# Optimization experiments

Hardware: AMD Instinct MI355X
Metric: run time of the kernel (lower is better)

Reference implementation:

```python
import jax, jax.numpy as jnp
import numpy as np

B, L, C, V = 16, 600, 256, 256
OUT_SEQ = 6000
KSZ = 5
DILATIONS = (1, 2, 4)
N_BLOCKS = 10
COND = 256  # speaker(128) + noise(128)
TEMP = 10.0
EPS = 1e-5


def _ccbn(x, cond, gw, gb, bw, bb):
    # x: (B, C, L); conditional batch-norm: per-channel stats over (batch, length),
    # gamma/beta predicted from condition vector.
    mu = jnp.mean(x, axis=(0, 2), keepdims=True)
    var = jnp.var(x, axis=(0, 2), keepdims=True)
    xn = (x - mu) * jax.lax.rsqrt(var + EPS)
    gamma = 1.0 + cond @ gw + gb  # (B, C)
    beta = cond @ bw + bb         # (B, C)
    return xn * gamma[:, :, None] + beta[:, :, None]


def _conv1d(x, w, b, dil=1):
    # x: (B, C_in, L); w: (C_out, C_in, K)
    y = jax.lax.conv_general_dilated(
        x, w, window_strides=(1,), padding='SAME', rhs_dilation=(dil,),
        dimension_numbers=('NCH', 'OIH', 'NCH'))
    return y + b[None, :, None]


def setup_inputs() -> dict:
    key = jax.random.key(0)
    ks = jax.random.split(key, 20)
    s = 0.02
    inp = {
        'inputs': jax.random.randint(ks[0], (B, L), 0, V),
        'speaker_embeddings': jax.random.normal(ks[1], (B, 128), jnp.float32),
        'noise': jax.random.normal(ks[2], (B, 128), jnp.float32),
        'emb': jax.random.normal(ks[3], (V, C), jnp.float32) * s,
        # 10 blocks x 3 dilated convs
        'conv_w': jax.random.normal(ks[4], (N_BLOCKS, 3, C, C, KSZ), jnp.float32) * s,
        'conv_b': jnp.zeros((N_BLOCKS, 3, C), jnp.float32),
        # CCBN projections per conv (gamma/beta from condition)
        'g_w': jax.random.normal(ks[5], (N_BLOCKS, 3, COND, C), jnp.float32) * s,
        'g_b': jnp.zeros((N_BLOCKS, 3, C), jnp.float32),
        'b_w': jax.random.normal(ks[6], (N_BLOCKS, 3, COND, C), jnp.float32) * s,
        'b_b': jnp.zeros((N_BLOCKS, 3, C), jnp.float32),
        # TokenLength head: 2 CCBNs + conv1 (256->256,k1) + conv2 (256->1,k1)
        'tl_g_w': jax.random.normal(ks[7], (2, COND, C), jnp.float32) * s,
        'tl_g_b': jnp.zeros((2, C), jnp.float32),
        'tl_b_w': jax.random.normal(ks[8], (2, COND, C), jnp.float32) * s,
        'tl_b_b': jnp.zeros((2, C), jnp.float32),
        'tl_conv1_w': jax.random.normal(ks[9], (C, C, 1), jnp.float32) * s,
        'tl_conv1_b': jnp.zeros((C,), jnp.float32),
        'tl_conv2_w': jax.random.normal(ks[10], (1, C, 1), jnp.float32) * s,
        'tl_conv2_b': jnp.zeros((1,), jnp.float32),
    }
    return inp


def reference(inputs, speaker_embeddings, noise, emb, conv_w, conv_b,
              g_w, g_b, b_w, b_b, tl_g_w, tl_g_b, tl_b_w, tl_b_b,
              tl_conv1_w, tl_conv1_b, tl_conv2_w, tl_conv2_b):
    cond = jnp.concatenate([speaker_embeddings, noise], axis=-1)  # (B, COND)
    x = emb[inputs]                    # (B, L, C)
    x = jnp.transpose(x, (0, 2, 1))    # (B, C, L)

    # 10 unaligned blocks: residual stacks of CCBN -> ReLU -> dilated conv
    for blk in range(N_BLOCKS):
        y = x
        for j, d in enumerate(DILATIONS):
            y = jax.nn.relu(_ccbn(y, cond, g_w[blk, j], g_b[blk, j], b_w[blk, j], b_b[blk, j]))
            y = _conv1d(y, conv_w[blk, j], conv_b[blk, j], dil=d)
        x = x + y
    unaligned = x  # (B, C, L)

    # TokenLength head
    t = jax.nn.relu(_ccbn(unaligned, cond, tl_g_w[0], tl_g_b[0], tl_b_w[0], tl_b_b[0]))
    t = _conv1d(t, tl_conv1_w, tl_conv1_b)
    t = jax.nn.relu(_ccbn(t, cond, tl_g_w[1], tl_g_b[1], tl_b_w[1], tl_b_b[1]))
    t = _conv1d(t, tl_conv2_w, tl_conv2_b)  # (B, 1, L)
    token_lengths = jax.nn.relu(t[:, 0, :])  # (B, L)

    token_ends = jnp.cumsum(token_lengths, axis=-1)        # (B, L)
    token_centers = token_ends - token_lengths / 2.0        # (B, L)
    aligned_lengths = token_ends

    out_pos = jnp.arange(OUT_SEQ, dtype=jnp.float32)         # (OUT,)
    diff = token_centers[:, None, :] - out_pos[None, :, None]  # (B, OUT, L)
    logits = -(diff * diff) / TEMP
    weights = jax.nn.softmax(logits, axis=-1)                # (B, OUT, L)

    feats = jnp.transpose(unaligned, (0, 2, 1))              # (B, L, C)
    aligned_features = jnp.einsum('bol,blc->boc', weights, feats)  # (B, OUT, C)
    return aligned_features, aligned_lengths
```

## Files before the change

### kernel.cpp

```cpp
#include <hip/hip_runtime.h>
#include <math.h>
#include <stdint.h>

#define EPSv 1e-5f

typedef short short8 __attribute__((ext_vector_type(8)));
typedef float floatx4 __attribute__((ext_vector_type(4)));

__device__ __forceinline__ unsigned short f2bf(float x) {
  unsigned u = __float_as_uint(x);
  unsigned r = (u + 0x7fffu + ((u >> 16) & 1u)) >> 16;
  return (unsigned short)r;
}

__device__ __forceinline__ void gld_lds16(const void* g, void* l) {
  __builtin_amdgcn_global_load_lds(
      (const __attribute__((address_space(1))) unsigned*)(uintptr_t)g,
      (__attribute__((address_space(3))) unsigned*)(uintptr_t)l,
      16, 0, 0);
}

__global__ __launch_bounds__(256) void k_gb_part(const float* __restrict__ spk,
                             const float* __restrict__ noise,
                             const float* __restrict__ g_w, const float* __restrict__ b_w,
                             const float* __restrict__ tl_g_w, const float* __restrict__ tl_b_w,
                             float* __restrict__ gpart, float* __restrict__ bpart) {
  __shared__ float condl[16][32];
  int i = blockIdx.x, ks = blockIdx.y;
  int t = threadIdx.x;
  for (int idx = t; idx < 512; idx += 256) {
    int b = idx >> 5, kk = idx & 31;
    int k = ks*32 + kk;
    condl[b][kk] = (k < 128) ? spk[b*128 + k] : noise[b*128 + k - 128];
  }
  __syncthreads();
  const float *gw, *bw;
  if (i < 30) { gw = g_w + (size_t)i*65536; bw = b_w + (size_t)i*65536; }
  else        { gw = tl_g_w + (size_t)(i-30)*65536; bw = tl_b_w + (size_t)(i-30)*65536; }
  int co = t;
  float g[16], bt[16];
  #pragma unroll
  for (int b = 0; b < 16; ++b) { g[b] = 0.f; bt[b] = 0.f; }
  for (int kk = 0; kk < 32; ++kk) {
    float gwv = gw[(size_t)(ks*32 + kk)*256 + co];
    float bwv = bw[(size_t)(ks*32 + kk)*256 + co];
    #pragma unroll
    for (int b = 0; b < 16; ++b) {
      float cv = condl[b][kk];
      g[b]  = fmaf(cv, gwv, g[b]);
      bt[b] = fmaf(cv, bwv, bt[b]);
    }
  }
  size_t base = ((size_t)(i*8 + ks)*16)*256 + co;
  #pragma unroll
  for (int b = 0; b < 16; ++b) {
    gpart[base + (size_t)b*256] = g[b];
    bpart[base + (size_t)b*256] = bt[b];
  }
}

__global__ void k_gb_red(const float* __restrict__ gpart, const float* __restrict__ bpart,
                         const float* __restrict__ g_b, const float* __restrict__ b_b,
                         const float* __restrict__ tl_g_b, const float* __restrict__ tl_b_b,
                         float* __restrict__ gammas, float* __restrict__ betas) {
  int idx = blockIdx.x*256 + threadIdx.x;
  int i = idx >> 12, rem = idx & 4095;
  int co = rem & 255;
  float gs = 0.f, bs = 0.f;
  #pragma unroll
  for (int ks = 0; ks < 8; ++ks) {
    size_t p = ((size_t)(i*8 + ks) << 12) + rem;
    gs += gpart[p];
    bs += bpart[p];
  }
  float gbias = (i < 30) ? g_b[i*256 + co] : tl_g_b[(i-30)*256 + co];
  float bbias = (i < 30) ? b_b[i*256 + co] : tl_b_b[(i-30)*256 + co];
  gammas[idx] = 1.0f + gs + gbias;
  betas [idx] = bs + bbias;
}

template<int TAPS>
__device__ __forceinline__ void wprep_body(const float* __restrict__ src,
                                           unsigned short* __restrict__ dst,
                                           int cotile, int chunk, int t) {
  int cow = t >> 2, ci8 = (t & 3) * 8;
  const float* s0 = src + ((size_t)(cotile*64 + cow)*256 + chunk*32 + ci8)*TAPS;
  float v[8*TAPS];
  #pragma unroll
  for (int i = 0; i < 8*TAPS; ++i) v[i] = s0[i];
  unsigned short* dblk = dst + (size_t)cotile*(8*TAPS*4096) + (size_t)chunk*(TAPS*4096);
  #pragma unroll
  for (int tap = 0; tap < TAPS; ++tap) {
    unsigned hi2[4], lo2[4];
    #pragma unroll
    for (int jj = 0; jj < 4; ++jj) {
      float a = v[(jj*2+0)*TAPS + tap], b = v[(jj*2+1)*TAPS + tap];
      unsigned short ha = f2bf(a), hb = f2bf(b);
      unsigned short la = f2bf(a - __uint_as_float((unsigned)ha << 16));
      unsigned short lb = f2bf(b - __uint_as_float((unsigned)hb << 16));
      hi2[jj] = (unsigned)ha | ((unsigned)hb << 16);
      lo2[jj] = (unsigned)la | ((unsigned)lb << 16);
    }
    uint4 H; H.x = hi2[0]; H.y = hi2[1]; H.z = hi2[2]; H.w = hi2[3];
    uint4 L; L.x = lo2[0]; L.y = lo2[1]; L.z = lo2[2]; L.w = lo2[3];
    *(uint4*)(dblk + (size_t)(tap*2)*2048 + cow*32 + ci8) = H;
    *(uint4*)(dblk + (size_t)(tap*2+1)*2048 + cow*32 + ci8) = L;
  }
}

__global__ __launch_bounds__(256) void k_wprep(const float* __restrict__ conv_w,
                                               const float* __restrict__ tl_c1_w,
                                               unsigned short* __restrict__ wp) {
  int cc = blockIdx.x;
  int cotile = blockIdx.y >> 3, chunk = blockIdx.y & 7;
  if (cc == 30) wprep_body<1>(tl_c1_w, wp + (size_t)30*655360, cotile, chunk, threadIdx.x);
  else          wprep_body<5>(conv_w + (size_t)cc*327680, wp + (size_t)cc*655360, cotile, chunk, threadIdx.x);
}

__global__ void k_embed2(const int* __restrict__ inp, const float* __restrict__ emb,
                         float* __restrict__ x, float* __restrict__ statp) {
  int bx = blockIdx.x;
  int c = threadIdx.x;
  int r0 = bx * 120;
  float s = 0.f, s2 = 0.f;
  for (int r = 0; r < 120; ++r) {
    int row = inp[r0 + r];
    float v = emb[(size_t)row*256 + c];
    x[(size_t)(r0 + r)*256 + c] = v;
    s += v; s2 = fmaf(v, v, s2);
  }
  statp[(size_t)bx*512 + c] = s;
  statp[(size_t)bx*512 + 256 + c] = s2;
}

__global__ __launch_bounds__(256) void k_norm(const float* __restrict__ z,
                      const float* __restrict__ statp,
                      const float* __restrict__ gam, const float* __restrict__ bet,
                      unsigned short* __restrict__ zn) {
  __shared__ float s_sc[32];
  __shared__ float s_sh[32];
  __shared__ float red[2][32][8];
  int b = blockIdx.x, chunk = blockIdx.y, sub = blockIdx.z;
  int t = threadIdx.x;
  {
    int ch = t >> 3, g = t & 7;
    int c = chunk*32 + ch;
    float s = 0.f, s2 = 0.f;
    for (int p = g; p < 80; p += 8) {
      s  += statp[(size_t)p*512 + c];
      s2 += statp[(size_t)p*512 + 256 + c];
    }
    red[0][ch][g] = s; red[1][ch][g] = s2;
  }
  __syncthreads();
  if (t < 32) {
    float s = 0.f, s2 = 0.f;
    #pragma unroll
    for (int g = 0; g < 8; ++g) { s += red[0][t][g]; s2 += red[1][t][g]; }
    int c = chunk*32 + t;
    float mu = s * (1.0f/9600.0f);
    float var = s2 * (1.0f/9600.0f) - mu*mu;
    float rs = rsqrtf(var + EPSv);
    float scale = rs * gam[b*256 + c];
    s_sc[t] = scale;
    s_sh[t] = fmaf(-mu, scale, bet[b*256 + c]);
  }
  __syncthreads();
  int srow = t >> 3, fq = t & 7;
  float4 sc4 = *(const float4*)&s_sc[fq*4];
  float4 sh4 = *(const float4*)&s_sh[fq*4];
  unsigned short* zh = zn + ((size_t)b*8 + chunk)*54400 + fq*4;
  unsigned short* zl = zh + 27200;
  const float* zb = z + (size_t)b*600*256 + chunk*32 + fq*4;
  int r0 = sub*68;
  #pragma unroll
  for (int i = 0; i < 3; ++i) {
    int rr = i*32 + srow;
    if (rr < 68) {
      int r = r0 + rr;
      int l = r - 8;
      uint2 vh; vh.x = 0u; vh.y = 0u;
      uint2 vl; vl.x = 0u; vl.y = 0u;
      if (l >= 0 && l < 600) {
        float4 zv = *(const float4*)&zb[(size_t)l*256];
        float v0 = fmaxf(fmaf(zv.x, sc4.x, sh4.x), 0.f);
        float v1 = fmaxf(fmaf(zv.y, sc4.y, sh4.y), 0.f);
        float v2 = fmaxf(fmaf(zv.z, sc4.z, sh4.z), 0.f);
        float v3 = fmaxf(fmaf(zv.w, sc4.w, sh4.w), 0.f);
        unsigned short h0 = f2bf(v0), h1 = f2bf(v1), h2 = f2bf(v2), h3 = f2bf(v3);
        unsigned short e0 = f2bf(v0 - __uint_as_float((unsigned)h0 << 16));
        unsigned short e1 = f2bf(v1 - __uint_as_float((unsigned)h1 << 16));
        unsigned short e2 = f2bf(v2 - __uint_as_float((unsigned)h2 << 16));
        unsigned short e3 = f2bf(v3 - __uint_as_float((unsigned)h3 << 16));
        vh.x = (unsigned)h0 | ((unsigned)h1 << 16);
        vh.y = (unsigned)h2 | ((unsigned)h3 << 16);
        vl.x = (unsigned)e0 | ((unsigned)e1 << 16);
        vl.y = (unsigned)e2 | ((unsigned)e3 << 16);
      }
      *(uint2*)&zh[(size_t)r*40] = vh;
      *(uint2*)&zl[(size_t)r*40] = vl;
    }
  }
}

template<int TAPS>
__global__ __launch_bounds__(256, 3) void k_convm(const unsigned short* __restrict__ zn,
                        float* __restrict__ out, float* __restrict__ statp,
                        const unsigned short* __restrict__ wpc,
                        const float* __restrict__ bias, int dil, int mode) {
  __shared__ __align__(16) unsigned short Zhi[2][6144];
  __shared__ __align__(16) unsigned short Zlo[2][6144];
  __shared__ float lsum[32];
  __shared__ float lsq[32];
  int t = threadIdx.x;
  int bx = blockIdx.x;
  int b  = bx / 5;
  int l0 = (bx % 5) * 128;
  int y = blockIdx.y;
  int co0 = y * 32;
  int cobase = (y & 1) * 32;
  int PAD = ((TAPS - 1)/2) * dil;
  int w = t >> 6, lane = t & 63;
  int lsub = (w & 1) * 64, cosub = (w >> 1) * 16;
  int quad = lane >> 4, nlan = lane & 15;
  if (t < 32) { lsum[t] = 0.f; lsq[t] = 0.f; }

  floatx4 acc[4];
  #pragma unroll
  for (int mt = 0; mt < 4; ++mt) acc[mt] = (floatx4){0.f,0.f,0.f,0.f};

  const unsigned short* zbase = zn + (size_t)b*435200 + (size_t)(l0 - PAD + 8)*40 + (size_t)lane*8;
  int ar[4];
  #pragma unroll
  for (int mt = 0; mt < 4; ++mt) ar[mt] = (lsub + mt*16 + nlan) * 40 + quad * 8;

  #define STAGEZ(ch, bf) do {                                             \
    const unsigned short* srcp = zbase + (size_t)(ch)*54400;              \
    for (int i = w; i < 24; i += 4) {                                     \
      int p = (i >= 12) ? 1 : 0;                                          \
      int k = i - p*12;                                                   \
      gld_lds16(srcp + p*27200 + k*512, (p ? Zlo[bf] : Zhi[bf]) + k*512); \
    }                                                                     \
  } while (0)

  STAGEZ(0, 0);
  __syncthreads();

  for (int chunk = 0; chunk < 8; ++chunk) {
    int cb = chunk & 1;
    if (chunk < 7) STAGEZ(chunk + 1, cb ^ 1);
    const unsigned short* pch = wpc + (size_t)((y >> 1)*8 + chunk) * (TAPS*4096);
    short8 bh[TAPS], bl[TAPS];
    int cw = (cobase + cosub + nlan)*32 + quad*8;
    #pragma unroll
    for (int tap = 0; tap < TAPS; ++tap) {
      bh[tap] = *(const short8*)(pch + (size_t)(tap*2)*2048 + cw);
      bl[tap] = *(const short8*)(pch + (size_t)(tap*2+1)*2048 + cw);
    }
    #pragma unroll
    for (int tap = 0; tap < TAPS; ++tap) {
      int sh = tap * dil * 40;
      #pragma unroll
      for (int mt = 0; mt < 4; ++mt) {
        short8 ah = *(const short8*)&Zhi[cb][ar[mt] + sh];
        short8 al = *(const short8*)&Zlo[cb][ar[mt] + sh];
        acc[mt] = __builtin_amdgcn_mfma_f32_16x16x32_bf16(ah, bh[tap], acc[mt], 0, 0, 0);
        acc[mt] = __builtin_amdgcn_mfma_f32_16x16x32_bf16(ah, bl[tap], acc[mt], 0, 0, 0);
        acc[mt] = __builtin_amdgcn_mfma_f32_16x16x32_bf16(al, bh[tap], acc[mt], 0, 0, 0);
      }
    }
    __syncthreads();
  }
  #undef STAGEZ

  float bsv = bias[co0 + cosub + nlan];
  float ssum = 0.f, ssq = 0.f;
  #pragma unroll
  for (int mt = 0; mt < 4; ++mt) {
    #pragma unroll
    for (int r = 0; r < 4; ++r) {
      int l = l0 + lsub + mt*16 + quad*4 + r;
      if (l < 600) {
        float v = acc[mt][r] + bsv;
        float* dst = &out[((size_t)(b*600 + l))*256 + co0 + cosub + nlan];
        if (mode) v += *dst;
        *dst = v;
        ssum += v;
        ssq = fmaf(v, v, ssq);
      }
    }
  }
  ssum += __shfl_xor(ssum, 16, 64);
  ssum += __shfl_xor(ssum, 32, 64);
  ssq  += __shfl_xor(ssq, 16, 64);
  ssq  += __shfl_xor(ssq, 32, 64);
  if (quad == 0) {
    atomicAdd(&lsum[cosub + nlan], ssum);
    atomicAdd(&lsq [cosub + nlan], ssq);
  }
  __syncthreads();
  if (t < 32) {
    statp[(size_t)bx*512 + co0 + t] = lsum[t];
    statp[(size_t)bx*512 + 256 + co0 + t] = lsq[t];
  }
}

__global__ void k_statred(const float* __restrict__ sp, float* __restrict__ dst) {
  int idx = blockIdx.x*256 + threadIdx.x;
  float s = 0.f;
  for (int p = 0; p < 80; ++p) s += sp[(size_t)p*512 + idx];
  dst[idx] = s;
}

__global__ void k_tl2(const float* __restrict__ z, const float* __restrict__ stat,
                      const float* __restrict__ gam, const float* __restrict__ bet,
                      const float* __restrict__ w2, const float* __restrict__ b2,
                      float* __restrict__ tl) {
  int t = threadIdx.x;
  int row = blockIdx.x * 4 + (t >> 6);
  int lane = t & 63;
  int b = row / 600;
  float4 s1 = *(const float4*)&stat[lane*4];
  float4 s2 = *(const float4*)&stat[256 + lane*4];
  float4 gm = *(const float4*)&gam[b*256 + lane*4];
  float4 bt = *(const float4*)&bet[b*256 + lane*4];
  float sc[4], sh[4];
  {
    float sv[4] = {s1.x, s1.y, s1.z, s1.w};
    float qv[4] = {s2.x, s2.y, s2.z, s2.w};
    float gv[4] = {gm.x, gm.y, gm.z, gm.w};
    float bv[4] = {bt.x, bt.y, bt.z, bt.w};
    #pragma unroll
    for (int i = 0; i < 4; ++i) {
      float mu = sv[i] * (1.0f/9600.0f);
      float var = qv[i] * (1.0f/9600.0f) - mu*mu;
      float rs = rsqrtf(var + EPSv);
      sc[i] = rs * gv[i];
      sh[i] = fmaf(-mu, sc[i], bv[i]);
    }
  }
  float4 zr = *(const float4*)&z[(size_t)row*256 + lane*4];
  float4 wr = *(const float4*)&w2[lane*4];
  float z0 = fmaxf(fmaf(zr.x, sc[0], sh[0]), 0.f);
  float z1 = fmaxf(fmaf(zr.y, sc[1], sh[1]), 0.f);
  float z2 = fmaxf(fmaf(zr.z, sc[2], sh[2]), 0.f);
  float z3 = fmaxf(fmaf(zr.w, sc[3], sh[3]), 0.f);
  float s = z0*wr.x + z1*wr.y + z2*wr.z + z3*wr.w;
  for (int m = 32; m >= 1; m >>= 1) s += __shfl_xor(s, m, 64);
  if (lane == 0) tl[row] = fmaxf(s + b2[0], 0.f);
}

__global__ void k_cumsum(const float* __restrict__ tl, float* __restrict__ centers,
                         float* __restrict__ out_len) {
  int b = blockIdx.x; int lane = threadIdx.x;
  float carry = 0.f;
  for (int ch = 0; ch < 10; ++ch) {
    int l = ch*64 + lane;
    float v = (l < 600) ? tl[b*600 + l] : 0.f;
    float s = v;
    #pragma unroll
    for (int off = 1; off < 64; off <<= 1) {
      float n = __shfl_up(s, off, 64);
      if (lane >= off) s += n;
    }
    float ends = carry + s;
    if (l < 600) {
      centers[b*600 + l] = ends - 0.5f*v;
      out_len[b*600 + l] = ends;
    }
    carry = __shfl(ends, 63, 64);
  }
}

__global__ void k_tobf16(const float* __restrict__ x, unsigned short* __restrict__ fbT) {
  __shared__ unsigned short T[64*66];
  int b = blockIdx.x, lt = blockIdx.y, ct = blockIdx.z;
  int t = threadIdx.x;
  int i4 = t >> 6;
  int j = t & 63;
  #pragma unroll
  for (int r = 0; r < 16; ++r) {
    int li = i4*16 + r;
    int l = lt*64 + li;
    float v = (l < 600) ? x[((size_t)(b*600 + l))*256 + ct*64 + j] : 0.f;
    T[j*66 + li] = f2bf(v);
  }
  __syncthreads();
  int row = t >> 2, seg = (t & 3) * 16;
  unsigned vv[8];
  #pragma unroll
  for (int k = 0; k < 8; ++k)
    vv[k] = *(const unsigned*)&T[row*66 + seg + k*2];
  size_t dsth = ((size_t)(b*256 + ct*64 + row))*640 + lt*64 + seg;
  unsigned* du = (unsigned*)fbT;
  uint4 a; a.x = vv[0]; a.y = vv[1]; a.z = vv[2]; a.w = vv[3];
  uint4 c4; c4.x = vv[4]; c4.y = vv[5]; c4.z = vv[6]; c4.w = vv[7];
  *(uint4*)(du + dsth/2) = a;
  *(uint4*)(du + dsth/2 + 4) = c4;
}

__global__ __launch_bounds__(256, 4) void k_align2(const unsigned short* __restrict__ fbT,
                        const float* __restrict__ centers, float* __restrict__ outp) {
  __shared__ float cen[600];
  __shared__ float mrow[64];
  __shared__ float isum[64];
  __shared__ unsigned short Wt[2][64*80];
  int b = blockIdx.x;
  int o0 = blockIdx.y * 64;
  int t = threadIdx.x;
  int wv = t >> 6, lane = t & 63;
  for (int i = t; i < 600; i += 256) cen[i] = centers[b*600 + i];
  __syncthreads();
  for (int rr = 0; rr < 16; ++rr) {
    int oi = wv*16 + rr;
    float opos = (float)(o0 + oi);
    float mx = -3.0e38f;
    for (int l = lane; l < 600; l += 64) {
      float d = cen[l] - opos;
      mx = fmaxf(mx, -d*d*0.1f);
    }
    #pragma unroll
    for (int mm = 32; mm >= 1; mm >>= 1) mx = fmaxf(mx, __shfl_xor(mx, mm, 64));
    if (lane == 0) mrow[oi] = mx;
  }
  __syncthreads();
  floatx4 acc[4][4];
  #pragma unroll
  for (int i = 0; i < 4; ++i)
    #pragma unroll
    for (int j = 0; j < 4; ++j)
      acc[i][j] = (floatx4){0.f, 0.f, 0.f, 0.f};
  int quad = lane >> 4;
  int nlan = lane & 15;
  int oi_w = t >> 2;
  int sbase = t & 3;
  float mo = mrow[oi_w];
  float opos_w = (float)(o0 + oi_w);
  float psum = 0.f;
  const unsigned short* srcb = fbT + ((size_t)b*256)*640;
  const unsigned short* fbl = srcb + (size_t)(wv*64 + nlan)*640 + quad*8;

  unsigned actm = 0;
  {
    float opos_l = (float)(o0 + lane);
    float mo_l = mrow[lane];
    for (int ch = 0; ch < 10; ++ch) {
      int lc0 = ch*64;
      int lc1 = (lc0 + 63 < 599) ? lc0 + 63 : 599;
      float clo = cen[lc0], chi = cen[lc1];
      float Do = fmaxf(fmaxf(clo - opos_l, opos_l - chi), 0.f);
      bool near = (fmaf(-Do*Do, 0.1f, -mo_l) >= -80.f);
      if (__ballot(near) != 0ull) actm |= (1u << ch);
    }
  }

  #define STAGE_WT(CH, BF) do {                                              \
    int lcs = (CH) * 64;                                                     \
    _Pragma("unroll")                                                        \
    for (int sidx = 0; sidx < 2; ++sidx) {                                   \
      int seg = sbase + sidx*4;                                              \
      unsigned pk[4];                                                        \
      _Pragma("unroll")                                                      \
      for (int jj = 0; jj < 8; jj += 2) {                                    \
        int li = lcs + seg*8 + jj;                                           \
        float e0 = 0.f, e1 = 0.f;                                            \
        if (li < 600)     { float d = cen[li] - opos_w;     e0 = __expf(-d*d*0.1f - mo); } \
        if (li + 1 < 600) { float d = cen[li + 1] - opos_w; e1 = __expf(-d*d*0.1f - mo); } \
        psum += e0 + e1;                                                     \
        pk[jj>>1] = (unsigned)f2bf(e0) | ((unsigned)f2bf(e1) << 16);         \
      }                                                                      \
      uint4 v; v.x = pk[0]; v.y = pk[1]; v.z = pk[2]; v.w = pk[3];           \
      *(uint4*)&Wt[BF][oi_w*80 + seg*8] = v;                                 \
    }                                                                        \
  } while (0)

  int ch = __ffs(actm) - 1;
  int buf = 0;
  STAGE_WT(ch, 0);
  __syncthreads();

  while (ch >= 0) {
    unsigned rem = actm & ~((2u << ch) - 1u);
    int nxt = rem ? (__ffs(rem) - 1) : -1;
    int lc0 = ch * 64;
    short8 bfr[2][4];
    #pragma unroll
    for (int ks = 0; ks < 2; ++ks)
      #pragma unroll
      for (int nt = 0; nt < 4; ++nt)
        bfr[ks][nt] = *(const short8*)(fbl + (size_t)nt*16*640 + lc0 + ks*32);
    if (nxt >= 0) STAGE_WT(nxt, buf ^ 1);
    #pragma unroll
    for (int ks = 0; ks < 2; ++ks) {
      int ko = ks*32 + quad*8;
      short8 af[4];
      #pragma unroll
      for (int mt = 0; mt < 4; ++mt)
        af[mt] = *(const short8*)&Wt[buf][(mt*16 + nlan)*80 + ko];
      #pragma unroll
      for (int mt = 0; mt < 4; ++mt)
        #pragma unroll
        for (int nt = 0; nt < 4; ++nt)
          acc[mt][nt] = __builtin_amdgcn_mfma_f32_16x16x32_bf16(af[mt], bfr[ks][nt], acc[mt][nt], 0, 0, 0);
    }
    __syncthreads();
    ch = nxt; buf ^= 1;
  }
  #undef STAGE_WT

  psum += __shfl_xor(psum, 1, 64);
  psum += __shfl_xor(psum, 2, 64);
  if ((t & 3) == 0) isum[oi_w] = 1.0f / psum;
  __syncthreads();
  #pragma unroll
  for (int mt = 0; mt < 4; ++mt) {
    #pragma unroll
    for (int r = 0; r < 4; ++r) {
      int oi = mt*16 + quad*4 + r;
      int o = o0 + oi;
      if (o < 6000) {
        float sc = isum[oi];
        #pragma unroll
        for (int nt = 0; nt < 4; ++nt) {
          int c = wv*64 + nt*16 + nlan;
          outp[((size_t)b*6000 + o)*256 + c] = acc[mt][nt][r] * sc;
        }
      }
    }
  }
}

extern "C" void kernel_launch(void* const* d_in, const int* in_sizes, int n_in,
                              void* d_out, int out_size, void* d_ws, size_t ws_size,
                              hipStream_t stream) {
  const int*   inputs = (const int*)  d_in[0];
  const float* spk    = (const float*)d_in[1];
  const float* noise  = (const float*)d_in[2];
  const float* emb    = (const float*)d_in[3];
  const float* conv_w = (const float*)d_in[4];
  const float* conv_b = (const float*)d_in[5];
  const float* g_w    = (const float*)d_in[6];
  const float* g_b    = (const float*)d_in[7];
  const float* b_w    = (const float*)d_in[8];
  const float* b_b    = (const float*)d_in[9];
  const float* tl_g_w = (const float*)d_in[10];
  const float* tl_g_b = (const float*)d_in[11];
  const float* tl_b_w = (const float*)d_in[12];
  const float* tl_b_b = (const float*)d_in[13];
  const float* tl_c1_w = (const float*)d_in[14];
  const float* tl_c1_b = (const float*)d_in[15];
  const float* tl_c2_w = (const float*)d_in[16];
  const float* tl_c2_b = (const float*)d_in[17];
  float* out = (float*)d_out;

  float* ws = (float*)d_ws;
  float* x       = ws;
  float* A       = x + 2457600;
  float* Bf      = A + 2457600;
  float* gammas  = Bf + 2457600;
  float* betas   = gammas + 131072;
  float* statp   = betas + 131072;
  float* stat31  = statp + 81920;
  float* tl      = stat31 + 512;
  float* cen     = tl + 9600;
  unsigned short* wp = (unsigned short*)(cen + 9600);
  unsigned short* Zn = wp + (size_t)31*655360;
  unsigned short* fbT = (unsigned short*)Bf;
  float* gpart = (float*)Zn;
  float* bpart = gpart + 1048576;

  k_wprep<<<dim3(31, 32), dim3(256), 0, stream>>>(conv_w, tl_c1_w, wp);
  k_gb_part<<<dim3(32, 8), dim3(256), 0, stream>>>(spk, noise, g_w, b_w,
      tl_g_w, tl_b_w, gpart, bpart);
  k_gb_red<<<dim3(512), dim3(256), 0, stream>>>(gpart, bpart, g_b, b_b,
      tl_g_b, tl_b_b, gammas, betas);
  k_embed2<<<dim3(80), dim3(256), 0, stream>>>(inputs, emb, x, statp);

  const int dils[3] = {1, 2, 4};
  for (int blk = 0; blk < 10; ++blk) {
    const float* srcs[3] = {x, A, Bf};
    float*       dsts[3] = {A, Bf, x};
    for (int j = 0; j < 3; ++j) {
      int idx = blk*3 + j;
      int mode = (j == 2) ? 1 : 0;
      k_norm<<<dim3(16, 8, 10), dim3(256), 0, stream>>>(srcs[j],
          statp, gammas + idx*4096, betas + idx*4096, Zn);
      k_convm<5><<<dim3(80, 8), dim3(256), 0, stream>>>(Zn, dsts[j],
          statp, wp + (size_t)idx*655360, conv_b + idx*256, dils[j], mode);
    }
  }
  k_norm<<<dim3(16, 8, 10), dim3(256), 0, stream>>>(x,
      statp, gammas + 30*4096, betas + 30*4096, Zn);
  k_convm<1><<<dim3(80, 8), dim3(256), 0, stream>>>(Zn, A,
      statp, wp + (size_t)30*655360, tl_c1_b, 1, 0);
  k_statred<<<dim3(2), dim3(256), 0, stream>>>(statp, stat31);
  k_tl2<<<dim3(2400), dim3(256), 0, stream>>>(A, stat31,
      gammas + 31*4096, betas + 31*4096, tl_c2_w, tl_c2_b, tl);
  k_cumsum<<<dim3(16), dim3(64), 0, stream>>>(tl, cen, out + 24576000);
  k_tobf16<<<dim3(16, 10, 4), dim3(256), 0, stream>>>(x, fbT);
  k_align2<<<dim3(16, 94), dim3(256), 0, stream>>>(fbT, cen, out);
}
```

Measured before the change: 1.527 ms.

## Finalize BN stats in last conv block; single-buffer conv LDS; coalesce align stores

Channel mean and rsqrt are now computed once by the last-finishing block of each conv or embed kernel, using an atomic counter. Each norm kernel then reads ready statistics instead of re-reducing 80 partials in every block, and the separate stat reduction kernel is removed. The conv kernel drops LDS double buffering for a single buffer and raises its occupancy hint to 4, which gives up overlap of loads with MFMA work. The align kernel stages output rows through shared memory so global stores are float4-coalesced.

```diff
diff --git a/kernel.cpp b/kernel.cpp
--- a/kernel.cpp
+++ b/kernel.cpp
@@ -19,6 +19,31 @@
       (__attribute__((address_space(3))) unsigned*)(uintptr_t)l,
       16, 0, 0);
 }
+
+__device__ __forceinline__ void stat_finalize(const float* __restrict__ statp,
+                                              float* __restrict__ statd,
+                                              int* __restrict__ cnt, int expect, int t) {
+  __threadfence();
+  __shared__ int isLast;
+  if (t == 0) isLast = (atomicAdd(cnt, 1) == expect - 1) ? 1 : 0;
+  __syncthreads();
+  if (isLast) {
+    __threadfence();
+    float s = 0.f, s2 = 0.f;
+    for (int p = 0; p < 80; ++p) {
+      s  += statp[(size_t)p*512 + t];
+      s2 += statp[(size_t)p*512 + 256 + t];
+    }
+    float mu = s * (1.0f/9600.0f);
+    float var = s2 * (1.0f/9600.0f) - mu*mu;
+    statd[t] = mu;
+    statd[256 + t] = rsqrtf(var + EPSv);
+    __threadfence();
+    if (t == 0) atomicExch(cnt, 0);
+  }
+}
+
+__global__ void k_zeroi(int* __restrict__ p) { if (threadIdx.x == 0) p[0] = 0; }
 
 __global__ __launch_bounds__(256) void k_gb_part(const float* __restrict__ spk,
                              const float* __restrict__ noise,
@@ -118,7 +143,8 @@
 }
 
 __global__ void k_embed2(const int* __restrict__ inp, const float* __restrict__ emb,
-                         float* __restrict__ x, float* __restrict__ statp) {
+                         float* __restrict__ x, float* __restrict__ statp,
+                         float* __restrict__ statd, int* __restrict__ cnt) {
   int bx = blockIdx.x;
   int c = threadIdx.x;
   int r0 = bx * 120;
@@ -131,44 +157,26 @@
   }
   statp[(size_t)bx*512 + c] = s;
   statp[(size_t)bx*512 + 256 + c] = s2;
+  stat_finalize(statp, statd, cnt, 80, c);
 }
 
 __global__ __launch_bounds__(256) void k_norm(const float* __restrict__ z,
-                      const float* __restrict__ statp,
+                      const float* __restrict__ statd,
                       const float* __restrict__ gam, const float* __restrict__ bet,
                       unsigned short* __restrict__ zn) {
-  __shared__ float s_sc[32];
-  __shared__ float s_sh[32];
-  __shared__ float red[2][32][8];
   int b = blockIdx.x, chunk = blockIdx.y, sub = blockIdx.z;
   int t = threadIdx.x;
-  {
-    int ch = t >> 3, g = t & 7;
-    int c = chunk*32 + ch;
-    float s = 0.f, s2 = 0.f;
-    for (int p = g; p < 80; p += 8) {
-      s  += statp[(size_t)p*512 + c];
-      s2 += statp[(size_t)p*512 + 256 + c];
-    }
-    red[0][ch][g] = s; red[1][ch][g] = s2;
-  }
-  __syncthreads();
-  if (t < 32) {
-    float s = 0.f, s2 = 0.f;
-    #pragma unroll
-    for (int g = 0; g < 8; ++g) { s += red[0][t][g]; s2 += red[1][t][g]; }
-    int c = chunk*32 + t;
-    float mu = s * (1.0f/9600.0f);
-    float var = s2 * (1.0f/9600.0f) - mu*mu;
-    float rs = rsqrtf(var + EPSv);
-    float scale = rs * gam[b*256 + c];
-    s_sc[t] = scale;
-    s_sh[t] = fmaf(-mu, scale, bet[b*256 + c]);
-  }
-  __syncthreads();
   int srow = t >> 3, fq = t & 7;
-  float4 sc4 = *(const float4*)&s_sc[fq*4];
-  float4 sh4 = *(const float4*)&s_sh[fq*4];
+  int c0 = chunk*32 + fq*4;
+  float4 mu4 = *(const float4*)&statd[c0];
+  float4 rs4 = *(const float4*)&statd[256 + c0];
+  float4 gm4 = *(const float4*)&gam[b*256 + c0];
+  float4 bt4 = *(const float4*)&bet[b*256 + c0];
+  float4 sc4, sh4;
+  sc4.x = rs4.x*gm4.x; sh4.x = fmaf(-mu4.x, sc4.x, bt4.x);
+  sc4.y = rs4.y*gm4.y; sh4.y = fmaf(-mu4.y, sc4.y, bt4.y);
+  sc4.z = rs4.z*gm4.z; sh4.z = fmaf(-mu4.z, sc4.z, bt4.z);
+  sc4.w = rs4.w*gm4.w; sh4.w = fmaf(-mu4.w, sc4.w, bt4.w);
   unsigned short* zh = zn + ((size_t)b*8 + chunk)*54400 + fq*4;
   unsigned short* zl = zh + 27200;
   const float* zb = z + (size_t)b*600*256 + chunk*32 + fq*4;
@@ -204,12 +212,13 @@
 }
 
 template<int TAPS>
-__global__ __launch_bounds__(256, 3) void k_convm(const unsigned short* __restrict__ zn,
+__global__ __launch_bounds__(256, 4) void k_convm(const unsigned short* __restrict__ zn,
                         float* __restrict__ out, float* __restrict__ statp,
+                        float* __restrict__ statd, int* __restrict__ cnt,
                         const unsigned short* __restrict__ wpc,
                         const float* __restrict__ bias, int dil, int mode) {
-  __shared__ __align__(16) unsigned short Zhi[2][6144];
-  __shared__ __align__(16) unsigned short Zlo[2][6144];
+  __shared__ __align__(16) unsigned short Zhi[6144];
+  __shared__ __align__(16) unsigned short Zlo[6144];
   __shared__ float lsum[32];
   __shared__ float lsq[32];
   int t = threadIdx.x;
@@ -234,21 +243,16 @@
   #pragma unroll
   for (int mt = 0; mt < 4; ++mt) ar[mt] = (lsub + mt*16 + nlan) * 40 + quad * 8;
 
-  #define STAGEZ(ch, bf) do {                                             \
-    const unsigned short* srcp = zbase + (size_t)(ch)*54400;              \
-    for (int i = w; i < 24; i += 4) {                                     \
-      int p = (i >= 12) ? 1 : 0;                                          \
-      int k = i - p*12;                                                   \
-      gld_lds16(srcp + p*27200 + k*512, (p ? Zlo[bf] : Zhi[bf]) + k*512); \
-    }                                                                     \
-  } while (0)
-
-  STAGEZ(0, 0);
-  __syncthreads();
-
   for (int chunk = 0; chunk < 8; ++chunk) {
-    int cb = chunk & 1;
-    if (chunk < 7) STAGEZ(chunk + 1, cb ^ 1);
+    if (chunk > 0) __syncthreads();
+    {
+      const unsigned short* srcp = zbase + (size_t)chunk*54400;
+      for (int i = w; i < 24; i += 4) {
+        int p = (i >= 12) ? 1 : 0;
+        int k = i - p*12;
+        gld_lds16(srcp + p*27200 + k*512, (p ? Zlo : Zhi) + k*512);
+      }
+    }
     const unsigned short* pch = wpc + (size_t)((y >> 1)*8 + chunk) * (TAPS*4096);
     short8 bh[TAPS], bl[TAPS];
     int cw = (cobase + cosub + nlan)*32 + quad*8;
@@ -257,21 +261,20 @@
       bh[tap] = *(const short8*)(pch + (size_t)(tap*2)*2048 + cw);
       bl[tap] = *(const short8*)(pch + (size_t)(tap*2+1)*2048 + cw);
     }
+    __syncthreads();
     #pragma unroll
     for (int tap = 0; tap < TAPS; ++tap) {
       int sh = tap * dil * 40;
       #pragma unroll
       for (int mt = 0; mt < 4; ++mt) {
-        short8 ah = *(const short8*)&Zhi[cb][ar[mt] + sh];
-        short8 al = *(const short8*)&Zlo[cb][ar[mt] + sh];
+        short8 ah = *(const short8*)&Zhi[ar[mt] + sh];
+        short8 al = *(const short8*)&Zlo[ar[mt] + sh];
         acc[mt] = __builtin_amdgcn_mfma_f32_16x16x32_bf16(ah, bh[tap], acc[mt], 0, 0, 0);
         acc[mt] = __builtin_amdgcn_mfma_f32_16x16x32_bf16(ah, bl[tap], acc[mt], 0, 0, 0);
         acc[mt] = __builtin_amdgcn_mfma_f32_16x16x32_bf16(al, bh[tap], acc[mt], 0, 0, 0);
       }
     }
-    __syncthreads();
-  }
-  #undef STAGEZ
+  }
 
   float bsv = bias[co0 + cosub + nlan];
   float ssum = 0.f, ssq = 0.f;
@@ -294,6 +297,7 @@
   ssum += __shfl_xor(ssum, 32, 64);
   ssq  += __shfl_xor(ssq, 16, 64);
   ssq  += __shfl_xor(ssq, 32, 64);
+  __syncthreads();
   if (quad == 0) {
     atomicAdd(&lsum[cosub + nlan], ssum);
     atomicAdd(&lsq [cosub + nlan], ssq);
@@ -303,16 +307,10 @@
     statp[(size_t)bx*512 + co0 + t] = lsum[t];
     statp[(size_t)bx*512 + 256 + co0 + t] = lsq[t];
   }
-}
-
-__global__ void k_statred(const float* __restrict__ sp, float* __restrict__ dst) {
-  int idx = blockIdx.x*256 + threadIdx.x;
-  float s = 0.f;
-  for (int p = 0; p < 80; ++p) s += sp[(size_t)p*512 + idx];
-  dst[idx] = s;
-}
-
-__global__ void k_tl2(const float* __restrict__ z, const float* __restrict__ stat,
+  stat_finalize(statp, statd, cnt, 640, t);
+}
+
+__global__ void k_tl2(const float* __restrict__ z, const float* __restrict__ statd,
                       const float* __restrict__ gam, const float* __restrict__ bet,
                       const float* __restrict__ w2, const float* __restrict__ b2,
                       float* __restrict__ tl) {
@@ -320,23 +318,20 @@
   int row = blockIdx.x * 4 + (t >> 6);
   int lane = t & 63;
   int b = row / 600;
-  float4 s1 = *(const float4*)&stat[lane*4];
-  float4 s2 = *(const float4*)&stat[256 + lane*4];
+  float4 mu4 = *(const float4*)&statd[lane*4];
+  float4 rs4 = *(const float4*)&statd[256 + lane*4];
   float4 gm = *(const float4*)&gam[b*256 + lane*4];
   float4 bt = *(const float4*)&bet[b*256 + lane*4];
   float sc[4], sh[4];
   {
-    float sv[4] = {s1.x, s1.y, s1.z, s1.w};
-    float qv[4] = {s2.x, s2.y, s2.z, s2.w};
+    float mv[4] = {mu4.x, mu4.y, mu4.z, mu4.w};
+    float rv[4] = {rs4.x, rs4.y, rs4.z, rs4.w};
     float gv[4] = {gm.x, gm.y, gm.z, gm.w};
     float bv[4] = {bt.x, bt.y, bt.z, bt.w};
     #pragma unroll
     for (int i = 0; i < 4; ++i) {
-      float mu = sv[i] * (1.0f/9600.0f);
-      float var = qv[i] * (1.0f/9600.0f) - mu*mu;
-      float rs = rsqrtf(var + EPSv);
-      sc[i] = rs * gv[i];
-      sh[i] = fmaf(-mu, sc[i], bv[i]);
+      sc[i] = rv[i] * gv[i];
+      sh[i] = fmaf(-mv[i], sc[i], bv[i]);
     }
   }
   float4 zr = *(const float4*)&z[(size_t)row*256 + lane*4];
@@ -405,6 +400,7 @@
   __shared__ float mrow[64];
   __shared__ float isum[64];
   __shared__ unsigned short Wt[2][64*80];
+  __shared__ float Ost[16*260];
   int b = blockIdx.x;
   int o0 = blockIdx.y * 64;
   int t = threadIdx.x;
@@ -512,20 +508,26 @@
   psum += __shfl_xor(psum, 2, 64);
   if ((t & 3) == 0) isum[oi_w] = 1.0f / psum;
   __syncthreads();
+
+  int orow = t >> 4, oseg = (t & 15) * 16;
   #pragma unroll
   for (int mt = 0; mt < 4; ++mt) {
+    if (mt > 0) __syncthreads();
     #pragma unroll
     for (int r = 0; r < 4; ++r) {
-      int oi = mt*16 + quad*4 + r;
-      int o = o0 + oi;
-      if (o < 6000) {
-        float sc = isum[oi];
-        #pragma unroll
-        for (int nt = 0; nt < 4; ++nt) {
-          int c = wv*64 + nt*16 + nlan;
-          outp[((size_t)b*6000 + o)*256 + c] = acc[mt][nt][r] * sc;
-        }
-      }
+      float sc = isum[mt*16 + quad*4 + r];
+      #pragma unroll
+      for (int nt = 0; nt < 4; ++nt)
+        Ost[(quad*4 + r)*260 + wv*64 + nt*16 + nlan] = acc[mt][nt][r] * sc;
+    }
+    __syncthreads();
+    int o = o0 + mt*16 + orow;
+    if (o < 6000) {
+      const float* src = &Ost[orow*260 + oseg];
+      float* dst = &outp[((size_t)b*6000 + o)*256 + oseg];
+      #pragma unroll
+      for (int q = 0; q < 4; ++q)
+        *(float4*)(dst + q*4) = *(const float4*)(src + q*4);
     }
   }
 }
@@ -560,8 +562,9 @@
   float* gammas  = Bf + 2457600;
   float* betas   = gammas + 131072;
   float* statp   = betas + 131072;
-  float* stat31  = statp + 81920;
-  float* tl      = stat31 + 512;
+  float* statd   = statp + 81920;
+  int*   cnt     = (int*)(statd + 512);
+  float* tl      = statd + 528;
   float* cen     = tl + 9600;
   unsigned short* wp = (unsigned short*)(cen + 9600);
   unsigned short* Zn = wp + (size_t)31*655360;
@@ -569,12 +572,13 @@
   float* gpart = (float*)Zn;
   float* bpart = gpart + 1048576;
 
+  k_zeroi<<<dim3(1), dim3(64), 0, stream>>>(cnt);
   k_wprep<<<dim3(31, 32), dim3(256), 0, stream>>>(conv_w, tl_c1_w, wp);
   k_gb_part<<<dim3(32, 8), dim3(256), 0, stream>>>(spk, noise, g_w, b_w,
       tl_g_w, tl_b_w, gpart, bpart);
   k_gb_red<<<dim3(512), dim3(256), 0, stream>>>(gpart, bpart, g_b, b_b,
       tl_g_b, tl_b_b, gammas, betas);
-  k_embed2<<<dim3(80), dim3(256), 0, stream>>>(inputs, emb, x, statp);
+  k_embed2<<<dim3(80), dim3(256), 0, stream>>>(inputs, emb, x, statp, statd, cnt);
 
   const int dils[3] = {1, 2, 4};
   for (int blk = 0; blk < 10; ++blk) {
@@ -584,17 +588,16 @@
       int idx = blk*3 + j;
       int mode = (j == 2) ? 1 : 0;
       k_norm<<<dim3(16, 8, 10), dim3(256), 0, stream>>>(srcs[j],
-          statp, gammas + idx*4096, betas + idx*4096, Zn);
+          statd, gammas + idx*4096, betas + idx*4096, Zn);
       k_convm<5><<<dim3(80, 8), dim3(256), 0, stream>>>(Zn, dsts[j],
-          statp, wp + (size_t)idx*655360, conv_b + idx*256, dils[j], mode);
+          statp, statd, cnt, wp + (size_t)idx*655360, conv_b + idx*256, dils[j], mode);
     }
   }
   k_norm<<<dim3(16, 8, 10), dim3(256), 0, stream>>>(x,
-      statp, gammas + 30*4096, betas + 30*4096, Zn);
+      statd, gammas + 30*4096, betas + 30*4096, Zn);
   k_convm<1><<<dim3(80, 8), dim3(256), 0, stream>>>(Zn, A,
-      statp, wp + (size_t)30*655360, tl_c1_b, 1, 0);
-  k_statred<<<dim3(2), dim3(256), 0, stream>>>(statp, stat31);
-  k_tl2<<<dim3(2400), dim3(256), 0, stream>>>(A, stat31,
+      statp, statd, cnt, wp + (size_t)30*655360, tl_c1_b, 1, 0);
+  k_tl2<<<dim3(2400), dim3(256), 0, stream>>>(A, statd,
       gammas + 31*4096, betas + 31*4096, tl_c2_w, tl_c2_b, tl);
   k_cumsum<<<dim3(16), dim3(64), 0, stream>>>(tl, cen, out + 24576000);
   k_tobf16<<<dim3(16, 10, 4), dim3(256), 0, stream>>>(x, fbT);
```

Result: slower. 3.165 ms (+107.3%).
